# Performance work log

Measured on AMD Instinct MI355X. Metric: run time of the kernel, lower is better.

The kernel has to match this reference:

```python
import jax, jax.numpy as jnp
import numpy as np

DIM = 1024
N_HEADS = 16
HEAD_DIM = DIM // N_HEADS


def setup_inputs() -> dict:
    key = jax.random.key(0)
    ks = jax.random.split(key, 5)
    B, L = 2, 2048
    q = jax.random.normal(ks[0], (B, L, DIM), dtype=jnp.float32)
    # nn.Linear weights: shape [out_features, in_features], applied as x @ W.T
    scale = 1.0 / np.sqrt(DIM)
    Wq = jax.random.normal(ks[1], (DIM, DIM), dtype=jnp.float32) * scale
    Wk = jax.random.normal(ks[2], (DIM, DIM), dtype=jnp.float32) * scale
    Wv = jax.random.normal(ks[3], (DIM, DIM), dtype=jnp.float32) * scale
    Wo = jax.random.normal(ks[4], (DIM, DIM), dtype=jnp.float32) * scale
    return {"q": q, "Wq": Wq, "Wk": Wk, "Wv": Wv, "Wo": Wo}


def reference(q, Wq, Wk, Wv, Wo):
    B, L, _ = q.shape
    kv = q  # self-attention (kv=None path)
    # projections: x @ W.T, then split heads: b l (h d) -> b h l d
    def split_heads(x):
        return x.reshape(B, L, N_HEADS, HEAD_DIM).transpose(0, 2, 1, 3)
    qh = split_heads(q @ Wq.T)
    kh = split_heads(kv @ Wk.T)
    vh = split_heads(kv @ Wv.T)
    # scaled dot-product attention; scale = sqrt(head_dim)
    scores = jnp.einsum('bhid,bhjd->bhij', qh, kh) / jnp.sqrt(
        jnp.asarray(HEAD_DIM, dtype=qh.dtype))
    attn = jax.nn.softmax(scores, axis=-1)
    out = jnp.einsum('bhij,bhjd->bhid', attn, vh)
    # b h l d -> b l (h d)
    out = out.transpose(0, 2, 1, 3).reshape(B, L, DIM)
    return out @ Wo.T
```

## Files before the change

### kernel.cpp

```cpp
#include <hip/hip_runtime.h>


#define DIMN 1024
#define NH 16
#define HD 64
#define BB 2
#define LL 2048

typedef float f32x4 __attribute__((ext_vector_type(4)));
typedef short s16x8 __attribute__((ext_vector_type(8)));

#define QSCALE 0.18033688011112042f

static __device__ __forceinline__ unsigned short f2bf(float f) {
  unsigned u = __float_as_uint(f);
  u += 0x7fffu + ((u >> 16) & 1u);
  return (unsigned short)(u >> 16);
}
static __device__ __forceinline__ unsigned packbf2(float lo, float hi) {
  return (unsigned)f2bf(lo) | ((unsigned)f2bf(hi) << 16);
}
static __device__ __forceinline__ float xexp2(float x) {
#if __has_builtin(__builtin_amdgcn_exp2f)
  return __builtin_amdgcn_exp2f(x);
#else
  return exp2f(x);
#endif
}
static __device__ __forceinline__ s16x8 cvt8(float4 a, float4 b) {
  s16x8 r;
  r[0] = (short)f2bf(a.x); r[1] = (short)f2bf(a.y);
  r[2] = (short)f2bf(a.z); r[3] = (short)f2bf(a.w);
  r[4] = (short)f2bf(b.x); r[5] = (short)f2bf(b.y);
  r[6] = (short)f2bf(b.z); r[7] = (short)f2bf(b.w);
  return r;
}
static __device__ __forceinline__ void gld16(const unsigned short* g,
                                             unsigned short* l) {
#if __has_builtin(__builtin_amdgcn_global_load_lds)
  __builtin_amdgcn_global_load_lds(
      (const __attribute__((address_space(1))) void*)g,
      (__attribute__((address_space(3))) void*)l, 16, 0, 0);
#else
  ((uint4*)l)[threadIdx.x & 63] = ((const uint4*)g)[0];
#endif
}

__global__ __launch_bounds__(256) void cvt_all(
    const float* __restrict__ X, const float* __restrict__ Wq,
    const float* __restrict__ Wk, const float* __restrict__ Wv,
    const float* __restrict__ Wo, unsigned short* __restrict__ out) {
  const int blk = blockIdx.x;
  const float* src;
  unsigned short* dst;
  size_t off;
  if (blk < 2048) {
    src = X; dst = out; off = (size_t)blk * 2048;
  } else {
    int s = (blk - 2048) >> 9;
    src = (s == 0) ? Wq : (s == 1) ? Wk : (s == 2) ? Wv : Wo;
    dst = out + ((size_t)1 << 22) + (size_t)s * (1u << 20);
    off = (size_t)((blk - 2048) & 511) * 2048;
  }
  size_t i = off + (size_t)threadIdx.x * 8;
  float4 v0 = *(const float4*)(src + i);
  float4 v1 = *(const float4*)(src + i + 4);
  uint4 o;
  o.x = packbf2(v0.x, v0.y); o.y = packbf2(v0.z, v0.w);
  o.z = packbf2(v1.x, v1.y); o.w = packbf2(v1.z, v1.w);
  *(uint4*)(dst + i) = o;
}

__global__ __launch_bounds__(256) void gemm_qkv(
    const unsigned short* __restrict__ Xb, const unsigned short* __restrict__ Wb,
    unsigned short* __restrict__ Qb, unsigned short* __restrict__ Kb,
    unsigned short* __restrict__ VT) {
  __shared__ __align__(16) unsigned short Al[128 * 32];
  __shared__ __align__(16) unsigned short Bl[128 * 32];
  const int m0 = blockIdx.x * 128;
  const int n0g = blockIdx.y * 128;
  const int sel = n0g >> 10;
  const int tid = threadIdx.x;
  const int w = tid >> 6, lane = tid & 63;
  const int c = lane & 15, quad = lane >> 4;
  const int wm = (w & 1) * 64, wn = (w >> 1) * 64;

  f32x4 zero = {0.f, 0.f, 0.f, 0.f};
  f32x4 acc[4][4];
#pragma unroll
  for (int i = 0; i < 4; ++i)
#pragma unroll
    for (int j = 0; j < 4; ++j) acc[i][j] = zero;

  const int srow = w * 32 + (lane >> 2);
  const int scol = (lane & 3) * 8;
  const unsigned short* gA = Xb + (size_t)(m0 + srow) * DIMN + scol;
  const unsigned short* gB = Wb + (size_t)(n0g + srow) * DIMN + scol;
  unsigned short* lA0 = Al + (w * 32) * 32;
  unsigned short* lA1 = Al + (w * 32 + 16) * 32;
  unsigned short* lB0 = Bl + (w * 32) * 32;
  unsigned short* lB1 = Bl + (w * 32 + 16) * 32;

  for (int k0 = 0; k0 < DIMN; k0 += 32) {
    __syncthreads();
    gld16(gA + k0, lA0);
    gld16(gA + k0 + 16 * DIMN, lA1);
    gld16(gB + k0, lB0);
    gld16(gB + k0 + 16 * DIMN, lB1);
    __syncthreads();
    s16x8 a[4], b[4];
#pragma unroll
    for (int i = 0; i < 4; ++i)
      a[i] = *(const s16x8*)&Al[(wm + i * 16 + c) * 32 + quad * 8];
#pragma unroll
    for (int j = 0; j < 4; ++j)
      b[j] = *(const s16x8*)&Bl[(wn + j * 16 + c) * 32 + quad * 8];
    if (sel != 2) {
#pragma unroll
      for (int i = 0; i < 4; ++i)
#pragma unroll
        for (int j = 0; j < 4; ++j)
          acc[i][j] = __builtin_amdgcn_mfma_f32_16x16x32_bf16(a[i], b[j], acc[i][j], 0, 0, 0);
    } else {
#pragma unroll
      for (int i = 0; i < 4; ++i)
#pragma unroll
        for (int j = 0; j < 4; ++j)
          acc[i][j] = __builtin_amdgcn_mfma_f32_16x16x32_bf16(b[j], a[i], acc[i][j], 0, 0, 0);
    }
  }

  const int n0 = n0g & 1023;
  if (sel != 2) {
    unsigned short* Out = (sel == 0) ? Qb : Kb;
    const float scale = (sel == 0) ? QSCALE : 1.0f;
#pragma unroll
    for (int i = 0; i < 4; ++i)
#pragma unroll
      for (int j = 0; j < 4; ++j)
#pragma unroll
        for (int r = 0; r < 4; ++r) {
          int row = m0 + wm + i * 16 + quad * 4 + r;
          int col = n0 + wn + j * 16 + c;
          Out[(((size_t)(row >> 11) * NH + (col >> 6)) * LL + (row & 2047)) * HD + (col & 63)] =
              f2bf(acc[i][j][r] * scale);
        }
  } else {
#pragma unroll
    for (int i = 0; i < 4; ++i)
#pragma unroll
      for (int j = 0; j < 4; ++j)
#pragma unroll
        for (int r = 0; r < 4; ++r) {
          int n = n0 + wn + j * 16 + quad * 4 + r;
          int m = m0 + wm + i * 16 + c;
          VT[(((size_t)(m >> 11) * NH + (n >> 6)) * HD + (n & 63)) * LL + (m & 2047)] =
              f2bf(acc[i][j][r]);
        }
  }
}

__global__ __launch_bounds__(256) void gemm_o(
    const unsigned short* __restrict__ A, const unsigned short* __restrict__ Wob,
    float* __restrict__ Out) {
  __shared__ __align__(16) unsigned short Al[128 * 32];
  __shared__ __align__(16) unsigned short Bl[64 * 32];
  const int m0 = blockIdx.x * 128;
  const int n0 = blockIdx.y * 64;
  const int tid = threadIdx.x;
  const int w = tid >> 6, lane = tid & 63;
  const int c = lane & 15, quad = lane >> 4;
  const int wm = (w & 1) * 64, wn = (w >> 1) * 32;

  f32x4 zero = {0.f, 0.f, 0.f, 0.f};
  f32x4 acc[4][2];
#pragma unroll
  for (int i = 0; i < 4; ++i)
#pragma unroll
    for (int j = 0; j < 2; ++j) acc[i][j] = zero;

  const int srow = w * 32 + (lane >> 2);
  const int brow = w * 16 + (lane >> 2);
  const int scol = (lane & 3) * 8;
  const unsigned short* gA = A + (size_t)(m0 + srow) * DIMN + scol;
  const unsigned short* gB = Wob + (size_t)(n0 + brow) * DIMN + scol;
  unsigned short* lA0 = Al + (w * 32) * 32;
  unsigned short* lA1 = Al + (w * 32 + 16) * 32;
  unsigned short* lB0 = Bl + (w * 16) * 32;

  for (int k0 = 0; k0 < DIMN; k0 += 32) {
    __syncthreads();
    gld16(gA + k0, lA0);
    gld16(gA + k0 + 16 * DIMN, lA1);
    gld16(gB + k0, lB0);
    __syncthreads();
    s16x8 a[4], b[2];
#pragma unroll
    for (int i = 0; i < 4; ++i)
      a[i] = *(const s16x8*)&Al[(wm + i * 16 + c) * 32 + quad * 8];
#pragma unroll
    for (int j = 0; j < 2; ++j)
      b[j] = *(const s16x8*)&Bl[(wn + j * 16 + c) * 32 + quad * 8];
#pragma unroll
    for (int i = 0; i < 4; ++i)
#pragma unroll
      for (int j = 0; j < 2; ++j)
        acc[i][j] = __builtin_amdgcn_mfma_f32_16x16x32_bf16(a[i], b[j], acc[i][j], 0, 0, 0);
  }

#pragma unroll
  for (int i = 0; i < 4; ++i)
#pragma unroll
    for (int j = 0; j < 2; ++j)
#pragma unroll
      for (int r = 0; r < 4; ++r)
        Out[(size_t)(m0 + wm + i * 16 + quad * 4 + r) * DIMN + n0 + wn + j * 16 + c] =
            acc[i][j][r];
}

__global__ __launch_bounds__(256) void attn3(
    const unsigned short* __restrict__ Qb, const unsigned short* __restrict__ Kb,
    const unsigned short* __restrict__ VT, unsigned short* __restrict__ AO) {
  __shared__ __align__(16) unsigned short Kl[64][72];
  __shared__ __align__(16) unsigned short Vtl[64][72];
  __shared__ __align__(16) unsigned short Pl[4][32][72];

  const int bh = blockIdx.y;
  const int tid = threadIdx.x;
  const int w = tid >> 6, lane = tid & 63;
  const int c = lane & 15, quad = lane >> 4;
  const int q0 = blockIdx.x * 128 + w * 32;

  const unsigned short* Qh = Qb + (size_t)bh * LL * HD;
  const unsigned short* Kh = Kb + (size_t)bh * LL * HD;
  const unsigned short* Vh = VT + (size_t)bh * HD * LL;

  s16x8 qf[2][2];
#pragma unroll
  for (int m = 0; m < 2; ++m)
#pragma unroll
    for (int f = 0; f < 2; ++f)
      qf[m][f] = *(const s16x8*)(Qh + (size_t)(q0 + m * 16 + c) * HD + f * 32 + quad * 8);

  f32x4 zero = {0.f, 0.f, 0.f, 0.f};
  f32x4 o[2][4];
  float lsum[2][4];
#pragma unroll
  for (int m = 0; m < 2; ++m)
#pragma unroll
    for (int r = 0; r < 4; ++r) lsum[m][r] = 0.f;
#pragma unroll
  for (int m = 0; m < 2; ++m)
#pragma unroll
    for (int dc = 0; dc < 4; ++dc) o[m][dc] = zero;

  const int krow = tid >> 2, kq = tid & 3;
  const int vd = tid >> 2, vh = (tid >> 1) & 1, vc0 = (tid & 1) * 8;

  for (int k0 = 0; k0 < LL; k0 += 64) {
    __syncthreads();
    {
      const unsigned short* ks = Kh + (size_t)(k0 + krow) * HD + kq * 16;
      uint4 ka = *(const uint4*)ks;
      uint4 kb2 = *(const uint4*)(ks + 8);
      const unsigned short* vs = Vh + (size_t)vd * LL + k0 + vh * 32 + vc0;
      uint4 va = *(const uint4*)vs;
      uint4 vb = *(const uint4*)(vs + 16);
      *(uint4*)&Kl[krow][kq * 16] = ka;
      *(uint4*)&Kl[krow][kq * 16 + 8] = kb2;
      const unsigned* ap = (const unsigned*)&va;
      const unsigned* bp = (const unsigned*)&vb;
      unsigned ov[8];
#pragma unroll
      for (int j = 0; j < 4; ++j) {
        ov[2 * j]     = __builtin_amdgcn_perm(bp[j], ap[j], 0x05040100u);
        ov[2 * j + 1] = __builtin_amdgcn_perm(bp[j], ap[j], 0x07060302u);
      }
      uint4 w0 = {ov[0], ov[1], ov[2], ov[3]};
      uint4 w1 = {ov[4], ov[5], ov[6], ov[7]};
      *(uint4*)&Vtl[vd][vh * 32 + vc0 * 2] = w0;
      *(uint4*)&Vtl[vd][vh * 32 + vc0 * 2 + 8] = w1;
    }
    __syncthreads();

    f32x4 s[2][4];
#pragma unroll
    for (int t = 0; t < 4; ++t) {
      s16x8 kfa = *(const s16x8*)&Kl[t * 16 + c][quad * 8];
      s16x8 kfb = *(const s16x8*)&Kl[t * 16 + c][32 + quad * 8];
#pragma unroll
      for (int m = 0; m < 2; ++m) {
        s[m][t] = __builtin_amdgcn_mfma_f32_16x16x32_bf16(qf[m][0], kfa, zero, 0, 0, 0);
        s[m][t] = __builtin_amdgcn_mfma_f32_16x16x32_bf16(qf[m][1], kfb, s[m][t], 0, 0, 0);
      }
    }

#pragma unroll
    for (int m = 0; m < 2; ++m)
#pragma unroll
      for (int r = 0; r < 4; ++r) {
        float p0 = xexp2(s[m][0][r]);
        float p1 = xexp2(s[m][1][r]);
        float p2 = xexp2(s[m][2][r]);
        float p3 = xexp2(s[m][3][r]);
        lsum[m][r] += (p0 + p1) + (p2 + p3);
        unsigned pk01 = __builtin_amdgcn_perm(__float_as_uint(p1), __float_as_uint(p0), 0x07060302u);
        unsigned pk23 = __builtin_amdgcn_perm(__float_as_uint(p3), __float_as_uint(p2), 0x07060302u);
        int row = m * 16 + quad * 4 + r;
        *(unsigned*)&Pl[w][row][2 * c] = pk01;
        *(unsigned*)&Pl[w][row][32 + 2 * c] = pk23;
      }
    asm volatile("s_waitcnt lgkmcnt(0)" ::: "memory");

#pragma unroll
    for (int kk = 0; kk < 2; ++kk) {
      s16x8 pf0 = *(const s16x8*)&Pl[w][c][kk * 32 + quad * 8];
      s16x8 pf1 = *(const s16x8*)&Pl[w][16 + c][kk * 32 + quad * 8];
#pragma unroll
      for (int dc = 0; dc < 4; ++dc) {
        s16x8 vf = *(const s16x8*)&Vtl[dc * 16 + c][kk * 32 + quad * 8];
        o[0][dc] = __builtin_amdgcn_mfma_f32_16x16x32_bf16(pf0, vf, o[0][dc], 0, 0, 0);
        o[1][dc] = __builtin_amdgcn_mfma_f32_16x16x32_bf16(pf1, vf, o[1][dc], 0, 0, 0);
      }
    }
  }

  const int bi = bh >> 4, h = bh & 15;
#pragma unroll
  for (int m = 0; m < 2; ++m)
#pragma unroll
    for (int r = 0; r < 4; ++r) {
      float l = lsum[m][r];
      l += __shfl_xor(l, 1);
      l += __shfl_xor(l, 2);
      l += __shfl_xor(l, 4);
      l += __shfl_xor(l, 8);
      float inv = 1.0f / l;
      int li = q0 + m * 16 + quad * 4 + r;
#pragma unroll
      for (int dc = 0; dc < 4; ++dc)
        AO[((size_t)bi * LL + li) * DIMN + h * HD + dc * 16 + c] = f2bf(o[m][dc][r] * inv);
    }
}

__global__ __launch_bounds__(64) void qkv_proj_f(
    const float* __restrict__ X, const float* __restrict__ Wq,
    const float* __restrict__ Wk, const float* __restrict__ Wv,
    unsigned short* __restrict__ Qb, unsigned short* __restrict__ Kb,
    unsigned short* __restrict__ VT) {
  const int m0 = blockIdx.x * 64;
  const int n0g = blockIdx.y * 64;
  const int sel = n0g >> 10;
  const int n0 = n0g & 1023;
  const float* W = (sel == 0) ? Wq : (sel == 1) ? Wk : Wv;
  const int lane = threadIdx.x;
  const int c = lane & 15, quad = lane >> 4;

  f32x4 zero = {0.f, 0.f, 0.f, 0.f};
  f32x4 acc[4][4];
#pragma unroll
  for (int i = 0; i < 4; ++i)
#pragma unroll
    for (int j = 0; j < 4; ++j) acc[i][j] = zero;

  const float* ab = X + (size_t)(m0 + c) * DIMN + quad * 8;
  const float* bb = W + (size_t)(n0 + c) * DIMN + quad * 8;

  for (int k0 = 0; k0 < DIMN; k0 += 32) {
    s16x8 a[4], b[4];
#pragma unroll
    for (int i = 0; i < 4; ++i) {
      const float* p = ab + i * 16 * DIMN + k0;
      a[i] = cvt8(*(const float4*)p, *(const float4*)(p + 4));
    }
#pragma unroll
    for (int j = 0; j < 4; ++j) {
      const float* p = bb + j * 16 * DIMN + k0;
      b[j] = cvt8(*(const float4*)p, *(const float4*)(p + 4));
    }
    if (sel != 2) {
#pragma unroll
      for (int i = 0; i < 4; ++i)
#pragma unroll
        for (int j = 0; j < 4; ++j)
          acc[i][j] = __builtin_amdgcn_mfma_f32_16x16x32_bf16(a[i], b[j], acc[i][j], 0, 0, 0);
    } else {
#pragma unroll
      for (int i = 0; i < 4; ++i)
#pragma unroll
        for (int j = 0; j < 4; ++j)
          acc[i][j] = __builtin_amdgcn_mfma_f32_16x16x32_bf16(b[j], a[i], acc[i][j], 0, 0, 0);
    }
  }

  if (sel != 2) {
    unsigned short* Out = (sel == 0) ? Qb : Kb;
    const float scale = (sel == 0) ? QSCALE : 1.0f;
#pragma unroll
    for (int i = 0; i < 4; ++i)
#pragma unroll
      for (int j = 0; j < 4; ++j)
#pragma unroll
        for (int r = 0; r < 4; ++r) {
          int row = m0 + i * 16 + quad * 4 + r;
          int nl = n0 + j * 16 + c;
          int bi = row >> 11, li = row & 2047;
          int h = nl >> 6, d = nl & 63;
          Out[(((size_t)bi * NH + h) * LL + li) * HD + d] = f2bf(acc[i][j][r] * scale);
        }
  } else {
#pragma unroll
    for (int i = 0; i < 4; ++i)
#pragma unroll
      for (int j = 0; j < 4; ++j)
#pragma unroll
        for (int r = 0; r < 4; ++r) {
          int n = n0 + j * 16 + quad * 4 + r;
          int l = m0 + i * 16 + c;
          int h = n >> 6, d = n & 63;
          int bi = l >> 11, li = l & 2047;
          VT[(((size_t)bi * NH + h) * HD + d) * LL + li] = f2bf(acc[i][j][r]);
        }
  }
}

__global__ __launch_bounds__(64) void o_proj_f(
    const unsigned short* __restrict__ A, const float* __restrict__ Wo,
    float* __restrict__ Out) {
  const int m0 = blockIdx.x * 64, n0 = blockIdx.y * 64;
  const int lane = threadIdx.x;
  const int c = lane & 15, quad = lane >> 4;

  f32x4 zero = {0.f, 0.f, 0.f, 0.f};
  f32x4 acc[4][4];
#pragma unroll
  for (int i = 0; i < 4; ++i)
#pragma unroll
    for (int j = 0; j < 4; ++j) acc[i][j] = zero;

  const unsigned short* ab = A + (size_t)(m0 + c) * DIMN + quad * 8;
  const float* bb = Wo + (size_t)(n0 + c) * DIMN + quad * 8;

  for (int k0 = 0; k0 < DIMN; k0 += 32) {
    s16x8 a[4], b[4];
#pragma unroll
    for (int i = 0; i < 4; ++i) a[i] = *(const s16x8*)(ab + i * 16 * DIMN + k0);
#pragma unroll
    for (int j = 0; j < 4; ++j) {
      const float* p = bb + j * 16 * DIMN + k0;
      b[j] = cvt8(*(const float4*)p, *(const float4*)(p + 4));
    }
#pragma unroll
    for (int i = 0; i < 4; ++i)
#pragma unroll
      for (int j = 0; j < 4; ++j)
        acc[i][j] = __builtin_amdgcn_mfma_f32_16x16x32_bf16(a[i], b[j], acc[i][j], 0, 0, 0);
  }

#pragma unroll
  for (int i = 0; i < 4; ++i)
#pragma unroll
    for (int j = 0; j < 4; ++j)
#pragma unroll
      for (int r = 0; r < 4; ++r)
        Out[(size_t)(m0 + i * 16 + quad * 4 + r) * DIMN + n0 + j * 16 + c] = acc[i][j][r];
}

extern "C" void kernel_launch(void* const* d_in, const int* in_sizes, int n_in,
                              void* d_out, int out_size, void* d_ws, size_t ws_size,
                              hipStream_t stream) {
  const float* X = (const float*)d_in[0];
  const float* Wq = (const float*)d_in[1];
  const float* Wk = (const float*)d_in[2];
  const float* Wv = (const float*)d_in[3];
  const float* Wo = (const float*)d_in[4];
  float* Out = (float*)d_out;

  const size_t M1 = (size_t)1 << 20;
  unsigned short* ws16 = (unsigned short*)d_ws;

  if (ws_size >= (size_t)48 * 1024 * 1024) {
    unsigned short* Xb = ws16;
    unsigned short* Wb = ws16 + 4 * M1;
    unsigned short* Qb = ws16 + 8 * M1;
    unsigned short* Kb = ws16 + 12 * M1;
    unsigned short* VT = ws16 + 16 * M1;
    unsigned short* AO = ws16 + 20 * M1;
    cvt_all<<<4096, 256, 0, stream>>>(X, Wq, Wk, Wv, Wo, ws16);
    gemm_qkv<<<dim3(32, 24), 256, 0, stream>>>(Xb, Wb, Qb, Kb, VT);
    attn3<<<dim3(LL / 128, BB * NH), 256, 0, stream>>>(Qb, Kb, VT, AO);
    gemm_o<<<dim3(32, 16), 256, 0, stream>>>(AO, Wb + 3 * M1, Out);
  } else {
    unsigned short* Qb = ws16;
    unsigned short* Kb = ws16 + 4 * M1;
    unsigned short* VT = ws16 + 8 * M1;
    unsigned short* AO = ws16 + 12 * M1;
    qkv_proj_f<<<dim3(64, 48), 64, 0, stream>>>(X, Wq, Wk, Wv, Qb, Kb, VT);
    attn3<<<dim3(LL / 128, BB * NH), 256, 0, stream>>>(Qb, Kb, VT, AO);
    o_proj_f<<<dim3(64, 16), 64, 0, stream>>>(AO, Wo, Out);
  }
}
```

Before: 201.0 us.

## Load K/V tiles via direct global-to-LDS with XOR swizzle and 128-key tiles

The attention kernel now stages K and V^T tiles with global_load_lds direct-to-LDS copies into XOR-swizzled unpadded layouts, and processes 128 keys per barrier pair instead of 64. The V projection writes V^T with an interleaved key order so the in-register perm shuffle when loading V can be dropped. This aims to cut VGPR round-trips, ALU permute work and barrier count. It doubles the K/V LDS footprint, which may lower occupancy, and the permuted V layout must match the P layout exactly.

```diff
diff --git a/kernel.cpp b/kernel.cpp
--- a/kernel.cpp
+++ b/kernel.cpp
@@ -45,6 +45,7 @@
   ((uint4*)l)[threadIdx.x & 63] = ((const uint4*)g)[0];
 #endif
 }
+
 
 __global__ __launch_bounds__(256) void cvt_all(
     const float* __restrict__ X, const float* __restrict__ Wq,
@@ -147,16 +148,18 @@
         }
   } else {
 #pragma unroll
-    for (int i = 0; i < 4; ++i)
+    for (int i = 0; i < 4; ++i) {
+      const int p64 = (i >> 1) * 32 + (i & 1);
 #pragma unroll
       for (int j = 0; j < 4; ++j)
 #pragma unroll
         for (int r = 0; r < 4; ++r) {
           int n = n0 + wn + j * 16 + quad * 4 + r;
-          int m = m0 + wm + i * 16 + c;
+          int m = m0 + wm + p64 + 2 * c;
           VT[(((size_t)(m >> 11) * NH + (n >> 6)) * HD + (n & 63)) * LL + (m & 2047)] =
               f2bf(acc[i][j][r]);
         }
+    }
   }
 }
 
@@ -218,11 +221,11 @@
             acc[i][j][r];
 }
 
-__global__ __launch_bounds__(256) void attn3(
+__global__ __launch_bounds__(256) void attn4(
     const unsigned short* __restrict__ Qb, const unsigned short* __restrict__ Kb,
     const unsigned short* __restrict__ VT, unsigned short* __restrict__ AO) {
-  __shared__ __align__(16) unsigned short Kl[64][72];
-  __shared__ __align__(16) unsigned short Vtl[64][72];
+  __shared__ __align__(16) unsigned short Kl[128 * 64];
+  __shared__ __align__(16) unsigned short Vtl[64 * 128];
   __shared__ __align__(16) unsigned short Pl[4][32][72];
 
   const int bh = blockIdx.y;
@@ -254,73 +257,69 @@
 #pragma unroll
     for (int dc = 0; dc < 4; ++dc) o[m][dc] = zero;
 
-  const int krow = tid >> 2, kq = tid & 3;
-  const int vd = tid >> 2, vh = (tid >> 1) & 1, vc0 = (tid & 1) * 8;
-
-  for (int k0 = 0; k0 < LL; k0 += 64) {
+  const int l8 = lane >> 3, p8 = lane & 7;
+  const unsigned short* gK = Kh + (size_t)(w * 8 + l8) * HD + ((p8 ^ l8) * 8);
+  unsigned short* lK = (unsigned short*)Kl + (w * 8) * 64;
+  const int l16 = lane >> 4, p16 = lane & 15;
+  const int vrow = w * 4 + l16;
+  const unsigned short* gV = Vh + (size_t)vrow * LL + ((p16 ^ vrow) * 8);
+  unsigned short* lV = (unsigned short*)Vtl + (w * 4) * 128;
+
+  const int kpa = (quad ^ (c & 7)) * 8;
+  const int kpb = ((quad + 4) ^ (c & 7)) * 8;
+
+  for (int k0 = 0; k0 < LL; k0 += 128) {
     __syncthreads();
-    {
-      const unsigned short* ks = Kh + (size_t)(k0 + krow) * HD + kq * 16;
-      uint4 ka = *(const uint4*)ks;
-      uint4 kb2 = *(const uint4*)(ks + 8);
-      const unsigned short* vs = Vh + (size_t)vd * LL + k0 + vh * 32 + vc0;
-      uint4 va = *(const uint4*)vs;
-      uint4 vb = *(const uint4*)(vs + 16);
-      *(uint4*)&Kl[krow][kq * 16] = ka;
-      *(uint4*)&Kl[krow][kq * 16 + 8] = kb2;
-      const unsigned* ap = (const unsigned*)&va;
-      const unsigned* bp = (const unsigned*)&vb;
-      unsigned ov[8];
-#pragma unroll
-      for (int j = 0; j < 4; ++j) {
-        ov[2 * j]     = __builtin_amdgcn_perm(bp[j], ap[j], 0x05040100u);
-        ov[2 * j + 1] = __builtin_amdgcn_perm(bp[j], ap[j], 0x07060302u);
+#pragma unroll
+    for (int s = 0; s < 4; ++s)
+      gld16(gK + (size_t)(k0 + s * 32) * HD, lK + s * 32 * 64);
+#pragma unroll
+    for (int s = 0; s < 4; ++s)
+      gld16(gV + (size_t)(s * 16) * LL + k0, lV + s * 16 * 128);
+    __syncthreads();
+
+#pragma unroll
+    for (int g = 0; g < 2; ++g) {
+      f32x4 s[2][4];
+#pragma unroll
+      for (int t4 = 0; t4 < 4; ++t4) {
+        const int t = g * 4 + t4;
+        s16x8 kfa = *(const s16x8*)&Kl[(t * 16 + c) * 64 + kpa];
+        s16x8 kfb = *(const s16x8*)&Kl[(t * 16 + c) * 64 + kpb];
+#pragma unroll
+        for (int m = 0; m < 2; ++m) {
+          s[m][t4] = __builtin_amdgcn_mfma_f32_16x16x32_bf16(qf[m][0], kfa, zero, 0, 0, 0);
+          s[m][t4] = __builtin_amdgcn_mfma_f32_16x16x32_bf16(qf[m][1], kfb, s[m][t4], 0, 0, 0);
+        }
       }
-      uint4 w0 = {ov[0], ov[1], ov[2], ov[3]};
-      uint4 w1 = {ov[4], ov[5], ov[6], ov[7]};
-      *(uint4*)&Vtl[vd][vh * 32 + vc0 * 2] = w0;
-      *(uint4*)&Vtl[vd][vh * 32 + vc0 * 2 + 8] = w1;
-    }
-    __syncthreads();
-
-    f32x4 s[2][4];
-#pragma unroll
-    for (int t = 0; t < 4; ++t) {
-      s16x8 kfa = *(const s16x8*)&Kl[t * 16 + c][quad * 8];
-      s16x8 kfb = *(const s16x8*)&Kl[t * 16 + c][32 + quad * 8];
-#pragma unroll
-      for (int m = 0; m < 2; ++m) {
-        s[m][t] = __builtin_amdgcn_mfma_f32_16x16x32_bf16(qf[m][0], kfa, zero, 0, 0, 0);
-        s[m][t] = __builtin_amdgcn_mfma_f32_16x16x32_bf16(qf[m][1], kfb, s[m][t], 0, 0, 0);
-      }
-    }
-
-#pragma unroll
-    for (int m = 0; m < 2; ++m)
-#pragma unroll
-      for (int r = 0; r < 4; ++r) {
-        float p0 = xexp2(s[m][0][r]);
-        float p1 = xexp2(s[m][1][r]);
-        float p2 = xexp2(s[m][2][r]);
-        float p3 = xexp2(s[m][3][r]);
-        lsum[m][r] += (p0 + p1) + (p2 + p3);
-        unsigned pk01 = __builtin_amdgcn_perm(__float_as_uint(p1), __float_as_uint(p0), 0x07060302u);
-        unsigned pk23 = __builtin_amdgcn_perm(__float_as_uint(p3), __float_as_uint(p2), 0x07060302u);
-        int row = m * 16 + quad * 4 + r;
-        *(unsigned*)&Pl[w][row][2 * c] = pk01;
-        *(unsigned*)&Pl[w][row][32 + 2 * c] = pk23;
-      }
-    asm volatile("s_waitcnt lgkmcnt(0)" ::: "memory");
-
-#pragma unroll
-    for (int kk = 0; kk < 2; ++kk) {
-      s16x8 pf0 = *(const s16x8*)&Pl[w][c][kk * 32 + quad * 8];
-      s16x8 pf1 = *(const s16x8*)&Pl[w][16 + c][kk * 32 + quad * 8];
-#pragma unroll
-      for (int dc = 0; dc < 4; ++dc) {
-        s16x8 vf = *(const s16x8*)&Vtl[dc * 16 + c][kk * 32 + quad * 8];
-        o[0][dc] = __builtin_amdgcn_mfma_f32_16x16x32_bf16(pf0, vf, o[0][dc], 0, 0, 0);
-        o[1][dc] = __builtin_amdgcn_mfma_f32_16x16x32_bf16(pf1, vf, o[1][dc], 0, 0, 0);
+#pragma unroll
+      for (int m = 0; m < 2; ++m)
+#pragma unroll
+        for (int r = 0; r < 4; ++r) {
+          float p0 = xexp2(s[m][0][r]);
+          float p1 = xexp2(s[m][1][r]);
+          float p2 = xexp2(s[m][2][r]);
+          float p3 = xexp2(s[m][3][r]);
+          lsum[m][r] += (p0 + p1) + (p2 + p3);
+          unsigned pk01 = __builtin_amdgcn_perm(__float_as_uint(p1), __float_as_uint(p0), 0x07060302u);
+          unsigned pk23 = __builtin_amdgcn_perm(__float_as_uint(p3), __float_as_uint(p2), 0x07060302u);
+          int row = m * 16 + quad * 4 + r;
+          *(unsigned*)&Pl[w][row][2 * c] = pk01;
+          *(unsigned*)&Pl[w][row][32 + 2 * c] = pk23;
+        }
+      asm volatile("s_waitcnt lgkmcnt(0)" ::: "memory");
+
+#pragma unroll
+      for (int kh = 0; kh < 2; ++kh) {
+        const int kk = g * 2 + kh;
+        s16x8 pf0 = *(const s16x8*)&Pl[w][c][kh * 32 + quad * 8];
+        s16x8 pf1 = *(const s16x8*)&Pl[w][16 + c][kh * 32 + quad * 8];
+#pragma unroll
+        for (int dc = 0; dc < 4; ++dc) {
+          s16x8 vf = *(const s16x8*)&Vtl[(dc * 16 + c) * 128 + (((kk * 4 + quad) ^ c) * 8)];
+          o[0][dc] = __builtin_amdgcn_mfma_f32_16x16x32_bf16(pf0, vf, o[0][dc], 0, 0, 0);
+          o[1][dc] = __builtin_amdgcn_mfma_f32_16x16x32_bf16(pf1, vf, o[1][dc], 0, 0, 0);
+        }
       }
     }
   }
@@ -410,17 +409,19 @@
         }
   } else {
 #pragma unroll
-    for (int i = 0; i < 4; ++i)
+    for (int i = 0; i < 4; ++i) {
+      const int p64 = (i >> 1) * 32 + (i & 1);
 #pragma unroll
       for (int j = 0; j < 4; ++j)
 #pragma unroll
         for (int r = 0; r < 4; ++r) {
           int n = n0 + j * 16 + quad * 4 + r;
-          int l = m0 + i * 16 + c;
+          int l = m0 + p64 + 2 * c;
           int h = n >> 6, d = n & 63;
           int bi = l >> 11, li = l & 2047;
           VT[(((size_t)bi * NH + h) * HD + d) * LL + li] = f2bf(acc[i][j][r]);
         }
+    }
   }
 }
 
@@ -488,7 +489,7 @@
     unsigned short* AO = ws16 + 20 * M1;
     cvt_all<<<4096, 256, 0, stream>>>(X, Wq, Wk, Wv, Wo, ws16);
     gemm_qkv<<<dim3(32, 24), 256, 0, stream>>>(Xb, Wb, Qb, Kb, VT);
-    attn3<<<dim3(LL / 128, BB * NH), 256, 0, stream>>>(Qb, Kb, VT, AO);
+    attn4<<<dim3(LL / 128, BB * NH), 256, 0, stream>>>(Qb, Kb, VT, AO);
     gemm_o<<<dim3(32, 16), 256, 0, stream>>>(AO, Wb + 3 * M1, Out);
   } else {
     unsigned short* Qb = ws16;
@@ -496,7 +497,7 @@
     unsigned short* VT = ws16 + 8 * M1;
     unsigned short* AO = ws16 + 12 * M1;
     qkv_proj_f<<<dim3(64, 48), 64, 0, stream>>>(X, Wq, Wk, Wv, Qb, Kb, VT);
-    attn3<<<dim3(LL / 128, BB * NH), 256, 0, stream>>>(Qb, Kb, VT, AO);
+    attn4<<<dim3(LL / 128, BB * NH), 256, 0, stream>>>(Qb, Kb, VT, AO);
     o_proj_f<<<dim3(64, 16), 64, 0, stream>>>(AO, Wo, Out);
   }
 }
```

New measurement: 196.9 us. -2.0%, faster.
